# Performance work log

Measured on AMD Instinct MI355X. Metric: run time of the kernel, lower is better.

The kernel has to match this reference:

```python
import jax, jax.numpy as jnp
import numpy as np

N_NODES = 50000
N_EDGES = 800000
N_GRAPHS = 64
EPS = 1e-5


def glorot(key, shape):
    fan_in, fan_out = shape[0], shape[1]
    lim = np.sqrt(6.0 / (fan_in + fan_out))
    return jax.random.uniform(key, shape, jnp.float32, -lim, lim)


def setup_inputs() -> dict:
    key = jax.random.key(0)
    ks = jax.random.split(key, 12)
    x = jax.random.normal(ks[0], (N_NODES, 1), jnp.float32)
    edge_index = jax.random.randint(ks[1], (2, N_EDGES), 0, N_NODES, jnp.int64)
    batch = jnp.sort(jax.random.randint(ks[2], (N_NODES,), 0, N_GRAPHS, jnp.int64))
    dims = [(1, 256), (256, 256), (256, 128)]
    params = {}
    for i, (di, do) in enumerate(dims):
        params[f"Wl{i}"] = glorot(ks[3 + 3 * i], (di, do))          # neighbor (lin_l) weight
        params[f"b{i}"] = jnp.zeros((do,), jnp.float32)              # lin_l bias
        params[f"Wr{i}"] = glorot(ks[4 + 3 * i], (di, do))           # root (lin_r) weight
    params["gamma"] = jnp.ones((128,), jnp.float32)
    params["beta"] = jnp.zeros((128,), jnp.float32)
    return {"x": x, "edge_index": edge_index, "batch": batch, **params}


def _sage_conv(x, src, dst, deg_inv, Wl, b, Wr):
    # mean-aggregate messages x[src] at dst, then lin_l(agg) + lin_r(x)
    agg = jax.ops.segment_sum(x[src], dst, num_segments=N_NODES) * deg_inv
    return agg @ Wl + b + x @ Wr


def reference(x, edge_index, batch, Wl0, b0, Wr0, Wl1, b1, Wr1, Wl2, b2, Wr2, gamma, beta):
    src, dst = edge_index[0], edge_index[1]
    deg = jax.ops.segment_sum(jnp.ones((N_EDGES,), x.dtype), dst, num_segments=N_NODES)
    deg_inv = (1.0 / jnp.maximum(deg, 1.0))[:, None]

    h = _sage_conv(x, src, dst, deg_inv, Wl0, b0, Wr0)
    h = jax.nn.relu(h)  # dropout is identity in eval mode
    h = _sage_conv(h, src, dst, deg_inv, Wl1, b1, Wr1)
    h = jax.nn.relu(h)
    h = _sage_conv(h, src, dst, deg_inv, Wl2, b2, Wr2)

    # global mean pool over graphs
    gsum = jax.ops.segment_sum(h, batch, num_segments=N_GRAPHS)
    gcnt = jax.ops.segment_sum(jnp.ones((N_NODES,), h.dtype), batch, num_segments=N_GRAPHS)
    g = gsum / jnp.maximum(gcnt, 1.0)[:, None]

    # LayerNorm over feature dim
    mu = jnp.mean(g, axis=-1, keepdims=True)
    var = jnp.var(g, axis=-1, keepdims=True)
    return (g - mu) * jax.lax.rsqrt(var + EPS) * gamma + beta
```

## Files before the change

### kernel.cpp

```cpp
#include <hip/hip_runtime.h>
#include <stdint.h>

#define NN 50000
#define NE 800000
#define NG 64
#define F1 256
#define NBK 196
#define NBS 392
#define EPB 2048
#define SCB 391
#define PB 256
#define PCH 196

typedef __bf16 bf16x8 __attribute__((ext_vector_type(8)));
typedef float f32x4 __attribute__((ext_vector_type(4)));

__device__ __forceinline__ float bf2f(unsigned int u) {
  union { float f; unsigned int i; } v; v.i = (u & 0xffffu) << 16; return v.f;
}
__device__ __forceinline__ unsigned short f2bf(float f) {
  union { float f; unsigned int i; } v; v.f = f;
  unsigned int r = v.i + 0x7fffu + ((v.i >> 16) & 1u);
  return (unsigned short)(r >> 16);
}
__device__ __forceinline__ float asf(unsigned int u) {
  union { unsigned int u; float f; } v; v.u = u; return v.f;
}
__device__ __forceinline__ unsigned int asu(float f) {
  union { float f; unsigned int u; } v; v.f = f; return v.u;
}

__global__ void k_bhist(const int* __restrict__ ei, int* __restrict__ btot_d,
                        int* __restrict__ btot_s) {
  __shared__ int lhd[NBK];
  __shared__ int lhs[NBS];
  for (int i = threadIdx.x; i < NBK; i += 256) lhd[i] = 0;
  for (int i = threadIdx.x; i < NBS; i += 256) lhs[i] = 0;
  __syncthreads();
  for (int e = blockIdx.x * blockDim.x + threadIdx.x; e < NE; e += gridDim.x * blockDim.x) {
    atomicAdd(&lhs[ei[e] >> 7], 1);
    atomicAdd(&lhd[ei[NE + e] >> 8], 1);
  }
  __syncthreads();
  for (int i = threadIdx.x; i < NBK; i += 256) atomicAdd(&btot_d[i], lhd[i]);
  for (int i = threadIdx.x; i < NBS; i += 256) atomicAdd(&btot_s[i], lhs[i]);
}

__global__ void k_bscan(const int* __restrict__ btot_d, const int* __restrict__ btot_s,
                        int* __restrict__ bbase, int* __restrict__ bcur,
                        int* __restrict__ sbase, int* __restrict__ scur,
                        int* __restrict__ rowp) {
  __shared__ int buf[512];
  int t = threadIdx.x;
  int v = (t < NBK) ? btot_d[t] : 0;
  buf[t] = v;
  __syncthreads();
  for (int off = 1; off < 512; off <<= 1) {
    int o = (t >= off) ? buf[t - off] : 0;
    __syncthreads();
    buf[t] += o;
    __syncthreads();
  }
  if (t < NBK) { bbase[t] = buf[t] - v; bcur[t] = buf[t] - v; }
  if (t == NBK - 1) bbase[NBK] = buf[t];
  __syncthreads();
  int v2 = (t < NBS) ? btot_s[t] : 0;
  buf[t] = v2;
  __syncthreads();
  for (int off = 1; off < 512; off <<= 1) {
    int o = (t >= off) ? buf[t - off] : 0;
    __syncthreads();
    buf[t] += o;
    __syncthreads();
  }
  if (t < NBS) { sbase[t] = buf[t] - v2; scur[t] = buf[t] - v2; }
  if (t == NBS - 1) sbase[NBS] = buf[t];
  if (t == 0) rowp[NN] = NE;
}

__global__ __launch_bounds__(256) void k_bscatter(
    const int* __restrict__ ei, const float* __restrict__ x,
    int* __restrict__ bcur, int* __restrict__ scur,
    uint2* __restrict__ recs, unsigned int* __restrict__ srecs) {
  __shared__ int lhd[NBK]; __shared__ int gbd[NBK];
  __shared__ int lhs[NBS]; __shared__ int gbs[NBS];
  int b = blockIdx.x, tid = threadIdx.x;
  int e0 = b * EPB;
  for (int i = tid; i < NBK; i += 256) lhd[i] = 0;
  for (int i = tid; i < NBS; i += 256) lhs[i] = 0;
  __syncthreads();
  unsigned int meta[8]; float xv[8]; int lofd[8]; int bkd[8]; int lofs[8]; int bks[8];
#pragma unroll
  for (int i = 0; i < 8; ++i) {
    int e = e0 + i * 256 + tid;
    bkd[i] = -1;
    if (e < NE) {
      int s = ei[e], d = ei[NE + e];
      bkd[i] = d >> 8; bks[i] = s >> 7;
      meta[i] = (unsigned int)s | ((unsigned int)d << 16);
      xv[i] = x[s];
      lofd[i] = atomicAdd(&lhd[bkd[i]], 1);
      lofs[i] = atomicAdd(&lhs[bks[i]], 1);
    }
  }
  __syncthreads();
  for (int i = tid; i < NBK; i += 256) gbd[i] = atomicAdd(&bcur[i], lhd[i]);
  for (int i = tid; i < NBS; i += 256) gbs[i] = atomicAdd(&scur[i], lhs[i]);
  __syncthreads();
#pragma unroll
  for (int i = 0; i < 8; ++i) {
    if (bkd[i] >= 0) {
      recs[gbd[bkd[i]] + lofd[i]] = make_uint2(meta[i], asu(xv[i]));
      unsigned int s = meta[i] & 0xFFFFu, d = meta[i] >> 16;
      srecs[gbs[bks[i]] + lofs[i]] = d | ((s & 127u) << 16);
    }
  }
}

__global__ __launch_bounds__(256) void k_csr(
    const uint2* __restrict__ recs, const int* __restrict__ bbase,
    const float* __restrict__ x, const int* __restrict__ batch,
    int* __restrict__ rowp, float2* __restrict__ ax,
    int* __restrict__ colx, uint2* __restrict__ dg) {
  __shared__ int cnt[256];
  __shared__ int sc[256];
  __shared__ float xs[256];
  int b = blockIdx.x, tid = threadIdx.x;
  int eb = bbase[b], ee = bbase[b + 1];
  cnt[tid] = 0;
  xs[tid] = 0.0f;
  __syncthreads();
  for (int e = eb + tid; e < ee; e += 256) {
    uint2 r = recs[e];
    int dl = (r.x >> 16) & 255;
    atomicAdd(&cnt[dl], 1);
    atomicAdd(&xs[dl], asf(r.y));
  }
  __syncthreads();
  sc[tid] = cnt[tid];
  __syncthreads();
  for (int off = 1; off < 256; off <<= 1) {
    int o = (tid >= off) ? sc[tid - off] : 0;
    __syncthreads();
    sc[tid] += o;
    __syncthreads();
  }
  int excl = sc[tid] - cnt[tid];
  int i = b * 256 + tid;
  float dinv = 1.0f / fmaxf((float)cnt[tid], 1.0f);
  if (i < NN) {
    rowp[i] = eb + excl;
    ax[i] = make_float2(xs[tid] * dinv, x[i]);
    dg[i] = make_uint2(asu(dinv), (unsigned int)batch[i]);
  }
  __syncthreads();
  sc[tid] = excl;
  __syncthreads();
  for (int e = eb + tid; e < ee; e += 256) {
    uint2 r = recs[e];
    int dl = (r.x >> 16) & 255;
    int s = r.x & 0xFFFF;
    int slot = atomicAdd(&sc[dl], 1);
    colx[eb + slot] = s;
  }
}

__global__ __launch_bounds__(256) void k_csc(
    const unsigned int* __restrict__ srecs, const int* __restrict__ sbase,
    const uint2* __restrict__ dg, float* __restrict__ wg) {
  __shared__ float wgrow[128][64];
  int b = blockIdx.x, tid = threadIdx.x;
  f32x4 zz = {0.f, 0.f, 0.f, 0.f};
  for (int j = tid; j < 2048; j += 256) ((f32x4*)wgrow)[j] = zz;
  __syncthreads();
  int eb = sbase[b], ee = sbase[b + 1];
  for (int e = eb + tid; e < ee; e += 256) {
    unsigned int r = srecs[e];
    int d = r & 0xFFFF;
    int sl = (r >> 16) & 127;
    uint2 t = dg[d];
    atomicAdd(&wgrow[sl][t.y], asf(t.x));
  }
  __syncthreads();
  int s0 = b * 128;
  for (int j = tid; j < 2048; j += 256) {
    int row = j >> 4, col = (j & 15) * 4;
    int s = s0 + row;
    if (s < NN) *(f32x4*)&wg[(size_t)s * NG + col] = *(const f32x4*)&wgrow[row][col];
  }
}

__global__ void k_cnt(const int* __restrict__ batch, int* __restrict__ cnt) {
  int g = threadIdx.x;
  if (g >= NG) return;
  int lo = 0, hi = NN;
  while (lo < hi) { int m = (lo + hi) >> 1; if (batch[m] < g) lo = m + 1; else hi = m; }
  int a = lo;
  lo = 0; hi = NN;
  while (lo < hi) { int m = (lo + hi) >> 1; if (batch[m] < g + 1) lo = m + 1; else hi = m; }
  cnt[g] = lo - a;
}

__global__ void k_axe(const int* __restrict__ colx, const float2* __restrict__ ax,
                      float2* __restrict__ axe) {
  int e = blockIdx.x * blockDim.x + threadIdx.x;
  if (e >= NE) return;
  axe[e] = ax[colx[e]];
}

__global__ void k_wprep(const float* __restrict__ Wl1, const float* __restrict__ Wr1,
                        unsigned short* __restrict__ wcat) {
  int t = blockIdx.x * blockDim.x + threadIdx.x;
  if (t >= 256 * 512) return;
  int n = t >> 9, k = t & 511;
  float v = (k < 256) ? Wl1[k * 256 + n] : Wr1[(k - 256) * 256 + n];
  wcat[t] = f2bf(v);
}

__global__ __launch_bounds__(256) void k_agg2(
    const float2* __restrict__ axe, const int* __restrict__ rowp,
    const float* __restrict__ Wl0, const float* __restrict__ b0,
    const float* __restrict__ Wr0, unsigned short* __restrict__ aggb) {
  int wid = threadIdx.x >> 6, lane = threadIdx.x & 63;
  int gw = blockIdx.x * 4 + wid;
  int tw = gridDim.x * 4;
  float wl[4], wr[4], bb[4];
#pragma unroll
  for (int k = 0; k < 4; ++k) {
    wl[k] = Wl0[lane * 4 + k];
    wr[k] = Wr0[lane * 4 + k];
    bb[k] = b0[lane * 4 + k];
  }
  for (int d = gw; d < NN; d += tw) {
    int beg = rowp[d], end = rowp[d + 1];
    float a[4] = {0.f, 0.f, 0.f, 0.f};
    float c[4] = {0.f, 0.f, 0.f, 0.f};
    int e = beg;
    for (; e + 3 < end; e += 4) {
      float2 v0 = axe[e], v1 = axe[e + 1], v2 = axe[e + 2], v3 = axe[e + 3];
#pragma unroll
      for (int k = 0; k < 4; ++k) {
        a[k] += fmaxf(fmaf(v0.x, wl[k], fmaf(v0.y, wr[k], bb[k])), 0.0f);
        c[k] += fmaxf(fmaf(v1.x, wl[k], fmaf(v1.y, wr[k], bb[k])), 0.0f);
        a[k] += fmaxf(fmaf(v2.x, wl[k], fmaf(v2.y, wr[k], bb[k])), 0.0f);
        c[k] += fmaxf(fmaf(v3.x, wl[k], fmaf(v3.y, wr[k], bb[k])), 0.0f);
      }
    }
    for (; e < end; ++e) {
      float2 v0 = axe[e];
#pragma unroll
      for (int k = 0; k < 4; ++k)
        a[k] += fmaxf(fmaf(v0.x, wl[k], fmaf(v0.y, wr[k], bb[k])), 0.0f);
    }
    float dinv = 1.0f / fmaxf((float)(end - beg), 1.0f);
    uint2 o;
    o.x = (unsigned int)f2bf((a[0] + c[0]) * dinv) | ((unsigned int)f2bf((a[1] + c[1]) * dinv) << 16);
    o.y = (unsigned int)f2bf((a[2] + c[2]) * dinv) | ((unsigned int)f2bf((a[3] + c[3]) * dinv) << 16);
    *(uint2*)(aggb + (size_t)d * F1 + lane * 4) = o;
  }
}

#define BM 128
#define BN 128
#define BK 32

__global__ __launch_bounds__(256) void k_gemm1(
    const unsigned short* __restrict__ aggb, const float2* __restrict__ ax,
    const unsigned short* __restrict__ wcat,
    const float* __restrict__ Wl0, const float* __restrict__ b0,
    const float* __restrict__ Wr0, const float* __restrict__ b1,
    unsigned short* __restrict__ h1b) {
  __shared__ unsigned short As[2][BM][BK];
  __shared__ unsigned short Bs[2][BN][BK];
  __shared__ float wl0s[256], wr0s[256], b0s[256];
  int bm = blockIdx.x, ct = blockIdx.y;
  int tid = threadIdx.x;
  int wid = tid >> 6, lane = tid & 63;
  int wr = wid >> 1, wc = wid & 1;
  int rc = lane & 15, kh = lane >> 4;
  int r0 = bm * BM;
  int srow = tid >> 1;
  int sslot = tid & 1;

  wl0s[tid] = Wl0[tid];
  wr0s[tid] = Wr0[tid];
  b0s[tid] = b0[tid];

  int rA = r0 + srow;
  bool rAok = rA < NN;
  float2 axv = rAok ? ax[rA] : make_float2(0.f, 0.f);

  f32x4 acc[4][4] = {};
  int4 ra0, ra1, rb0, rb1;

#define LOAD_A(kt)                                                             \
  do {                                                                         \
    ra0 = make_int4(0, 0, 0, 0); ra1 = make_int4(0, 0, 0, 0);                  \
    if (rAok) {                                                                \
      const int4* s_ = (const int4*)(aggb + (size_t)rA * F1 + (kt) * BK + sslot * 16); \
      ra0 = s_[0]; ra1 = s_[1];                                                \
    }                                                                          \
  } while (0)

#define LOAD_B(kt)                                                             \
  do {                                                                         \
    const int4* t_ = (const int4*)(wcat + (size_t)(ct * BN + srow) * 512 + (kt) * BK + sslot * 16); \
    rb0 = t_[0]; rb1 = t_[1];                                                  \
  } while (0)

#define COMP_A(kt)                                                             \
  do {                                                                         \
    int j0_ = ((kt) - 8) * BK + sslot * 16;                                    \
    unsigned int w_[8];                                                        \
    _Pragma("unroll") for (int q = 0; q < 8; ++q) {                            \
      int j_ = j0_ + 2 * q;                                                    \
      float f0_ = fmaxf(fmaf(axv.x, wl0s[j_], fmaf(axv.y, wr0s[j_], b0s[j_])), 0.0f); \
      float f1_ = fmaxf(fmaf(axv.x, wl0s[j_ + 1], fmaf(axv.y, wr0s[j_ + 1], b0s[j_ + 1])), 0.0f); \
      w_[q] = (unsigned int)f2bf(f0_) | ((unsigned int)f2bf(f1_) << 16);       \
    }                                                                          \
    ra0 = make_int4(w_[0], w_[1], w_[2], w_[3]);                               \
    ra1 = make_int4(w_[4], w_[5], w_[6], w_[7]);                               \
  } while (0)

#define WRITE_AB(buf)                                                          \
  do {                                                                         \
    int sw_ = (srow >> 1) & 3;                                                 \
    int ws0_ = (2 * sslot) ^ sw_;                                              \
    int ws1_ = (2 * sslot + 1) ^ sw_;                                          \
    *(int4*)&As[buf][srow][ws0_ * 8] = ra0;                                    \
    *(int4*)&As[buf][srow][ws1_ * 8] = ra1;                                    \
    *(int4*)&Bs[buf][srow][ws0_ * 8] = rb0;                                    \
    *(int4*)&Bs[buf][srow][ws1_ * 8] = rb1;                                    \
  } while (0)

  LOAD_B(0);
  LOAD_A(0);
  WRITE_AB(0);
  __syncthreads();
  int cur = 0;
  for (int kt = 0; kt < 16; ++kt) {
    if (kt < 15) {
      LOAD_B(kt + 1);
      if (kt + 1 < 8) LOAD_A(kt + 1);
    }
    bf16x8 af[4], bfr[4];
#pragma unroll
    for (int mf = 0; mf < 4; ++mf) {
      int row = wr * 64 + mf * 16 + rc;
      int sl = kh ^ ((row >> 1) & 3);
      af[mf] = *(const bf16x8*)&As[cur][row][sl * 8];
    }
#pragma unroll
    for (int nf = 0; nf < 4; ++nf) {
      int row = wc * 64 + nf * 16 + rc;
      int sl = kh ^ ((row >> 1) & 3);
      bfr[nf] = *(const bf16x8*)&Bs[cur][row][sl * 8];
    }
#pragma unroll
    for (int nf = 0; nf < 4; ++nf)
#pragma unroll
      for (int mf = 0; mf < 4; ++mf)
        acc[nf][mf] = __builtin_amdgcn_mfma_f32_16x16x32_bf16(bfr[nf], af[mf], acc[nf][mf], 0, 0, 0);
    if (kt < 15) {
      if (kt + 1 >= 8) COMP_A(kt + 1);
      WRITE_AB(cur ^ 1);
    }
    __syncthreads();
    cur ^= 1;
  }
#undef LOAD_A
#undef LOAD_B
#undef COMP_A
#undef WRITE_AB

#pragma unroll
  for (int nf = 0; nf < 4; ++nf) {
    int c0 = ct * BN + wc * 64 + nf * 16 + kh * 4;
    float4 bb = *(const float4*)(b1 + c0);
#pragma unroll
    for (int mf = 0; mf < 4; ++mf) {
      int r = r0 + wr * 64 + mf * 16 + rc;
      if (r < NN) {
        f32x4 v = acc[nf][mf];
        unsigned int lo = (unsigned int)f2bf(fmaxf(v[0] + bb.x, 0.0f)) |
                          ((unsigned int)f2bf(fmaxf(v[1] + bb.y, 0.0f)) << 16);
        unsigned int hi = (unsigned int)f2bf(fmaxf(v[2] + bb.z, 0.0f)) |
                          ((unsigned int)f2bf(fmaxf(v[3] + bb.w, 0.0f)) << 16);
        *(uint2*)(h1b + (size_t)r * F1 + c0) = make_uint2(lo, hi);
      }
    }
  }
}

__global__ __launch_bounds__(512) void k_pool2(
    const unsigned short* __restrict__ h1b, const float* __restrict__ wg,
    const int* __restrict__ batch, float* __restrict__ zpart,
    float* __restrict__ p1) {
  __shared__ float h1s[32][256];
  __shared__ float wgs[32][64];
  int b = blockIdx.x, tid = threadIdx.x;
  int s0 = b * PCH;
  int lim = min(s0 + PCH, NN);
  int gq = tid >> 6;
  int fq = tid & 63;
  int col = tid & 255;
  int half = tid >> 8;
  f32x4 acc[8] = {};
  float pac = 0.0f;
  int curg = -1;
  for (int t0 = 0; t0 < PCH; t0 += 32) {
    int base = s0 + t0;
    {
      int r = tid >> 4;
      int c0 = (tid & 15) * 16;
      int s = base + r;
      uint4 va = make_uint4(0, 0, 0, 0), vb = make_uint4(0, 0, 0, 0);
      if (s < lim) {
        va = *(const uint4*)(h1b + (size_t)s * F1 + c0);
        vb = *(const uint4*)(h1b + (size_t)s * F1 + c0 + 8);
      }
      float* dst = &h1s[r][c0];
      unsigned int u[8] = {va.x, va.y, va.z, va.w, vb.x, vb.y, vb.z, vb.w};
#pragma unroll
      for (int q = 0; q < 8; ++q) {
        dst[2 * q] = bf2f(u[q]);
        union { float f; unsigned int i; } hi; hi.i = u[q] & 0xffff0000u;
        dst[2 * q + 1] = hi.f;
      }
    }
    {
      int r = tid >> 4;
      int c0 = (tid & 15) * 4;
      int s = base + r;
      float4 v = make_float4(0.f, 0.f, 0.f, 0.f);
      if (s < lim) v = *(const float4*)(wg + (size_t)s * NG + c0);
      *(float4*)&wgs[r][c0] = v;
    }
    __syncthreads();
    int rows = min(32, lim - base);
    for (int k = 0; k < rows; ++k) {
      f32x4 hv = *(const f32x4*)&h1s[k][fq << 2];
      f32x4 w0 = *(const f32x4*)&wgs[k][gq << 3];
      f32x4 w1 = *(const f32x4*)&wgs[k][(gq << 3) + 4];
#pragma unroll
      for (int i = 0; i < 4; ++i) acc[i] += w0[i] * hv;
#pragma unroll
      for (int i = 0; i < 4; ++i) acc[4 + i] += w1[i] * hv;
    }
    int kend = min(half * 16 + 16, rows);
    for (int k = half * 16; k < kend; ++k) {
      int g = batch[base + k];
      if (g != curg) {
        if (curg >= 0) atomicAdd(&p1[curg * F1 + col], pac);
        pac = 0.0f;
        curg = g;
      }
      pac += h1s[k][col];
    }
    __syncthreads();
  }
  if (curg >= 0) atomicAdd(&p1[curg * F1 + col], pac);
  float* zp = zpart + ((size_t)b * 64 + gq * 8) * F1 + (fq << 2);
#pragma unroll
  for (int i = 0; i < 8; ++i) *(f32x4*)(zp + (size_t)i * F1) = acc[i];
}

__global__ void k_zred(const float* __restrict__ zpart, float* __restrict__ z) {
  int g = blockIdx.x, q = blockIdx.y, t = threadIdx.x;
  float a = 0.0f;
  for (int b = q * 64; b < q * 64 + 64; ++b)
    a += zpart[((size_t)b * 64 + g) * F1 + t];
  atomicAdd(&z[g * F1 + t], a);
}

__global__ void k_final(const float* __restrict__ z, const float* __restrict__ p1,
                        const int* __restrict__ cnt,
                        const float* __restrict__ Wl2, const float* __restrict__ b2,
                        const float* __restrict__ Wr2, const float* __restrict__ gamma,
                        const float* __restrict__ beta, float* __restrict__ out) {
  __shared__ float s1[128], s2[128];
  int g = blockIdx.x, j = threadIdx.x;
  float invc = 1.0f / fmaxf((float)cnt[g], 1.0f);
  float acc = 0.0f;
  for (int k = 0; k < 256; ++k) {
    acc += z[g * 256 + k] * Wl2[k * 128 + j] + p1[g * 256 + k] * Wr2[k * 128 + j];
  }
  acc = acc * invc + b2[j];
  s1[j] = acc; s2[j] = acc * acc;
  __syncthreads();
  for (int off = 64; off > 0; off >>= 1) {
    if (j < off) { s1[j] += s1[j + off]; s2[j] += s2[j + off]; }
    __syncthreads();
  }
  float mu = s1[0] / 128.0f;
  float var = s2[0] / 128.0f - mu * mu;
  out[g * 128 + j] = (acc - mu) * rsqrtf(var + 1e-5f) * gamma[j] + beta[j];
}

extern "C" void kernel_launch(void* const* d_in, const int* in_sizes, int n_in,
                              void* d_out, int out_size, void* d_ws, size_t ws_size,
                              hipStream_t stream) {
  const float* x = (const float*)d_in[0];
  const int* ei = (const int*)d_in[1];
  const int* batch = (const int*)d_in[2];
  const float* Wl0 = (const float*)d_in[3];
  const float* b0 = (const float*)d_in[4];
  const float* Wr0 = (const float*)d_in[5];
  const float* Wl1 = (const float*)d_in[6];
  const float* b1 = (const float*)d_in[7];
  const float* Wr1 = (const float*)d_in[8];
  const float* Wl2 = (const float*)d_in[9];
  const float* b2 = (const float*)d_in[10];
  const float* Wr2 = (const float*)d_in[11];
  const float* gamma = (const float*)d_in[12];
  const float* beta = (const float*)d_in[13];
  float* out = (float*)d_out;

  char* p = (char*)d_ws;
  auto alloc = [&](size_t bytes) {
    char* r = p;
    p += (bytes + 511) & ~(size_t)511;
    return r;
  };
  unsigned short* h1b = (unsigned short*)alloc((size_t)NN * F1 * 2);
  unsigned short* aggb = (unsigned short*)alloc((size_t)NN * F1 * 2);
  float2* axe = (float2*)alloc((size_t)NE * 8);
  int* rowp = (int*)alloc((size_t)(NN + 1) * 4);
  float2* ax = (float2*)alloc((size_t)NN * 8);
  uint2* dg = (uint2*)alloc((size_t)NN * 8);
  int* cnt = (int*)alloc((size_t)NG * 4);
  float* z = (float*)alloc((size_t)NG * F1 * 4);
  float* p1 = (float*)alloc((size_t)NG * F1 * 4);
  unsigned short* wcat = (unsigned short*)alloc((size_t)256 * 512 * 2);
  int* btot_d = (int*)alloc((size_t)NBK * 4);
  int* btot_s = (int*)alloc((size_t)NBS * 4);
  int* bbase = (int*)alloc((size_t)(NBK + 1) * 4);
  int* bcur = (int*)alloc((size_t)NBK * 4);
  int* sbase = (int*)alloc((size_t)(NBS + 1) * 4);
  int* scur = (int*)alloc((size_t)NBS * 4);
  float* wg = (float*)alloc((size_t)NN * NG * 4);
  uint2* recs = (uint2*)aggb;
  unsigned int* srecs = (unsigned int*)(aggb + (size_t)NE * 4);
  int* colx = (int*)(aggb + (size_t)NE * 6);
  float* zpart = (float*)aggb;

  hipMemsetAsync(btot_d, 0, (size_t)NBK * 4, stream);
  hipMemsetAsync(btot_s, 0, (size_t)NBS * 4, stream);
  hipMemsetAsync(p1, 0, (size_t)NG * F1 * 4, stream);
  hipMemsetAsync(z, 0, (size_t)NG * F1 * 4, stream);

  k_bhist<<<256, 256, 0, stream>>>(ei, btot_d, btot_s);
  k_bscan<<<1, 512, 0, stream>>>(btot_d, btot_s, bbase, bcur, sbase, scur, rowp);
  k_bscatter<<<SCB, 256, 0, stream>>>(ei, x, bcur, scur, recs, srecs);
  k_csr<<<NBK, 256, 0, stream>>>(recs, bbase, x, batch, rowp, ax, colx, dg);
  k_csc<<<NBS, 256, 0, stream>>>(srecs, sbase, dg, wg);
  k_cnt<<<1, 64, 0, stream>>>(batch, cnt);
  k_axe<<<(NE + 255) / 256, 256, 0, stream>>>(colx, ax, axe);
  k_wprep<<<(256 * 512 + 255) / 256, 256, 0, stream>>>(Wl1, Wr1, wcat);
  k_agg2<<<2048, 256, 0, stream>>>(axe, rowp, Wl0, b0, Wr0, aggb);
  dim3 gg(391, 2);
  k_gemm1<<<gg, 256, 0, stream>>>(aggb, ax, wcat, Wl0, b0, Wr0, b1, h1b);
  k_pool2<<<PB, 512, 0, stream>>>(h1b, wg, batch, zpart, p1);
  dim3 zg(NG, 4);
  k_zred<<<zg, 256, 0, stream>>>(zpart, z);
  k_final<<<NG, 128, 0, stream>>>(z, p1, cnt, Wl2, b2, Wr2, gamma, beta, out);
}
```

Before: 218.6 us.

## Fuse root-pooling into GEMM epilogue and run graph-weight pooling on MFMA

The GEMM epilogue now writes h1 transposed (feature-major, swizzled through LDS) and accumulates the per-graph root sum p1 directly with shuffles and atomics, removing that work from the pool kernel. The per-node graph weights from k_csc are stored transposed as a split bf16 hi/lo pair so the z = wg^T·h1 reduction can run as a bf16 MFMA GEMM in a new k_poolmm kernel, replacing the scalar FMA k_pool2. This targets the FP32 scalar pooling cost and the extra pass over h1. In exchange it adds a padded node dimension, extra epilogue atomics, and h1 rounding to bf16 in the pooling product.

Measured after the change: 223.2 us. 2.1% more time.

```diff
diff --git a/kernel.cpp b/kernel.cpp
--- a/kernel.cpp
+++ b/kernel.cpp
@@ -5,12 +5,13 @@
 #define NE 800000
 #define NG 64
 #define F1 256
+#define NNP 50176
 #define NBK 196
 #define NBS 392
 #define EPB 2048
 #define SCB 391
-#define PB 256
-#define PCH 196
+#define PCHUNKS 112
+#define PKC 448
 
 typedef __bf16 bf16x8 __attribute__((ext_vector_type(8)));
 typedef float f32x4 __attribute__((ext_vector_type(4)));
@@ -167,11 +168,10 @@
 
 __global__ __launch_bounds__(256) void k_csc(
     const unsigned int* __restrict__ srecs, const int* __restrict__ sbase,
-    const uint2* __restrict__ dg, float* __restrict__ wg) {
-  __shared__ float wgrow[128][64];
+    const uint2* __restrict__ dg, unsigned int* __restrict__ wgT2u) {
+  __shared__ float wgrow[128 * 65];
   int b = blockIdx.x, tid = threadIdx.x;
-  f32x4 zz = {0.f, 0.f, 0.f, 0.f};
-  for (int j = tid; j < 2048; j += 256) ((f32x4*)wgrow)[j] = zz;
+  for (int i = tid; i < 128 * 65; i += 256) wgrow[i] = 0.0f;
   __syncthreads();
   int eb = sbase[b], ee = sbase[b + 1];
   for (int e = eb + tid; e < ee; e += 256) {
@@ -179,14 +179,19 @@
     int d = r & 0xFFFF;
     int sl = (r >> 16) & 127;
     uint2 t = dg[d];
-    atomicAdd(&wgrow[sl][t.y], asf(t.x));
-  }
-  __syncthreads();
-  int s0 = b * 128;
-  for (int j = tid; j < 2048; j += 256) {
-    int row = j >> 4, col = (j & 15) * 4;
-    int s = s0 + row;
-    if (s < NN) *(f32x4*)&wg[(size_t)s * NG + col] = *(const f32x4*)&wgrow[row][col];
+    atomicAdd(&wgrow[sl * 65 + t.y], asf(t.x));
+  }
+  __syncthreads();
+  int s0u = b * 64;
+  int k = tid & 63;
+  for (int rr = 0; rr < 16; ++rr) {
+    int g = rr * 4 + (tid >> 6);
+    float w0 = wgrow[(2 * k) * 65 + g];
+    float w1 = wgrow[(2 * k + 1) * 65 + g];
+    unsigned short h0 = f2bf(w0), h1v = f2bf(w1);
+    unsigned short l0 = f2bf(w0 - bf2f(h0)), l1 = f2bf(w1 - bf2f(h1v));
+    wgT2u[(size_t)g * (NNP / 2) + s0u + k] = (unsigned int)h0 | ((unsigned int)h1v << 16);
+    wgT2u[(size_t)(64 + g) * (NNP / 2) + s0u + k] = (unsigned int)l0 | ((unsigned int)l1 << 16);
   }
 }
 
@@ -269,10 +274,17 @@
     const unsigned short* __restrict__ wcat,
     const float* __restrict__ Wl0, const float* __restrict__ b0,
     const float* __restrict__ Wr0, const float* __restrict__ b1,
-    unsigned short* __restrict__ h1b) {
-  __shared__ unsigned short As[2][BM][BK];
-  __shared__ unsigned short Bs[2][BN][BK];
-  __shared__ float wl0s[256], wr0s[256], b0s[256];
+    const int* __restrict__ batch, float* __restrict__ p1,
+    unsigned short* __restrict__ h1T) {
+  __shared__ unsigned char SMEM[35840];
+  typedef unsigned short ush;
+  ush (*As)[BM][BK] = (ush (*)[BM][BK])SMEM;
+  ush (*Bs)[BN][BK] = (ush (*)[BN][BK])(SMEM + 16384);
+  float* wl0s = (float*)(SMEM + 32768);
+  float* wr0s = wl0s + 256;
+  float* b0s = wl0s + 512;
+  ush* Ts = (ush*)SMEM;
+
   int bm = blockIdx.x, ct = blockIdx.y;
   int tid = threadIdx.x;
   int wid = tid >> 6, lane = tid & 63;
@@ -373,103 +385,107 @@
 #undef COMP_A
 #undef WRITE_AB
 
+  int gv[4];
+#pragma unroll
+  for (int mf = 0; mf < 4; ++mf) {
+    int s = r0 + wr * 64 + mf * 16 + rc;
+    gv[mf] = (s < NN) ? batch[s] : -1;
+  }
+  int g0 = 0, g1 = -1;
+  if (r0 < NN) {
+    g0 = batch[r0];
+    g1 = batch[min(r0 + 127, NN - 1)];
+  }
+
 #pragma unroll
   for (int nf = 0; nf < 4; ++nf) {
-    int c0 = ct * BN + wc * 64 + nf * 16 + kh * 4;
-    float4 bb = *(const float4*)(b1 + c0);
+    int c0l = wc * 64 + nf * 16 + kh * 4;
+    float4 bbq = *(const float4*)(b1 + ct * BN + c0l);
+    float bbv[4] = {bbq.x, bbq.y, bbq.z, bbq.w};
+    float v[4][4];
+#pragma unroll
+    for (int mf = 0; mf < 4; ++mf)
+#pragma unroll
+      for (int j = 0; j < 4; ++j)
+        v[mf][j] = fmaxf(acc[nf][mf][j] + bbv[j], 0.0f);
 #pragma unroll
     for (int mf = 0; mf < 4; ++mf) {
-      int r = r0 + wr * 64 + mf * 16 + rc;
-      if (r < NN) {
-        f32x4 v = acc[nf][mf];
-        unsigned int lo = (unsigned int)f2bf(fmaxf(v[0] + bb.x, 0.0f)) |
-                          ((unsigned int)f2bf(fmaxf(v[1] + bb.y, 0.0f)) << 16);
-        unsigned int hi = (unsigned int)f2bf(fmaxf(v[2] + bb.z, 0.0f)) |
-                          ((unsigned int)f2bf(fmaxf(v[3] + bb.w, 0.0f)) << 16);
-        *(uint2*)(h1b + (size_t)r * F1 + c0) = make_uint2(lo, hi);
+      int s_loc = wr * 64 + mf * 16 + rc;
+#pragma unroll
+      for (int j = 0; j < 4; ++j) {
+        int f_loc = c0l + j;
+        Ts[f_loc * 128 + (s_loc ^ ((f_loc & 7) << 3))] = f2bf(v[mf][j]);
       }
     }
-  }
-}
-
-__global__ __launch_bounds__(512) void k_pool2(
-    const unsigned short* __restrict__ h1b, const float* __restrict__ wg,
-    const int* __restrict__ batch, float* __restrict__ zpart,
-    float* __restrict__ p1) {
-  __shared__ float h1s[32][256];
-  __shared__ float wgs[32][64];
-  int b = blockIdx.x, tid = threadIdx.x;
-  int s0 = b * PCH;
-  int lim = min(s0 + PCH, NN);
-  int gq = tid >> 6;
-  int fq = tid & 63;
-  int col = tid & 255;
-  int half = tid >> 8;
+    for (int g = g0; g <= g1; ++g) {
+#pragma unroll
+      for (int j = 0; j < 4; ++j) {
+        float s = 0.f;
+#pragma unroll
+        for (int mf = 0; mf < 4; ++mf) s += (gv[mf] == g) ? v[mf][j] : 0.f;
+        s += __shfl_xor(s, 1); s += __shfl_xor(s, 2);
+        s += __shfl_xor(s, 4); s += __shfl_xor(s, 8);
+        if (rc == 0 && s != 0.f) atomicAdd(&p1[g * F1 + ct * BN + c0l + j], s);
+      }
+    }
+  }
+  __syncthreads();
+  {
+    int f_loc = tid >> 1;
+    int sh = (tid & 1) * 64;
+    size_t rowoff = (size_t)(ct * BN + f_loc) * NNP + (size_t)bm * BM;
+#pragma unroll
+    for (int q = 0; q < 8; ++q) {
+      int s_l = sh + q * 8;
+      int4 vv = *(const int4*)&Ts[f_loc * 128 + (s_l ^ ((f_loc & 7) << 3))];
+      *(int4*)(h1T + rowoff + s_l) = vv;
+    }
+  }
+}
+
+__global__ __launch_bounds__(512) void k_poolmm(
+    const unsigned short* __restrict__ h1T, const unsigned short* __restrict__ wgT2,
+    float* __restrict__ zpart) {
+  int bid = blockIdx.x;
+  int c = bid % PCHUNKS, fh = bid / PCHUNKS;
+  int tid = threadIdx.x;
+  int w = tid >> 6, lane = tid & 63, rc = lane & 15, kh = lane >> 4;
+  size_t soff = (size_t)c * PKC + kh * 8;
+  const unsigned short* bp = h1T + (size_t)(fh * 128 + w * 16 + rc) * NNP + soff;
+  const unsigned short* ap = wgT2 + (size_t)rc * NNP + soff;
   f32x4 acc[8] = {};
-  float pac = 0.0f;
-  int curg = -1;
-  for (int t0 = 0; t0 < PCH; t0 += 32) {
-    int base = s0 + t0;
-    {
-      int r = tid >> 4;
-      int c0 = (tid & 15) * 16;
-      int s = base + r;
-      uint4 va = make_uint4(0, 0, 0, 0), vb = make_uint4(0, 0, 0, 0);
-      if (s < lim) {
-        va = *(const uint4*)(h1b + (size_t)s * F1 + c0);
-        vb = *(const uint4*)(h1b + (size_t)s * F1 + c0 + 8);
-      }
-      float* dst = &h1s[r][c0];
-      unsigned int u[8] = {va.x, va.y, va.z, va.w, vb.x, vb.y, vb.z, vb.w};
-#pragma unroll
-      for (int q = 0; q < 8; ++q) {
-        dst[2 * q] = bf2f(u[q]);
-        union { float f; unsigned int i; } hi; hi.i = u[q] & 0xffff0000u;
-        dst[2 * q + 1] = hi.f;
-      }
-    }
-    {
-      int r = tid >> 4;
-      int c0 = (tid & 15) * 4;
-      int s = base + r;
-      float4 v = make_float4(0.f, 0.f, 0.f, 0.f);
-      if (s < lim) v = *(const float4*)(wg + (size_t)s * NG + c0);
-      *(float4*)&wgs[r][c0] = v;
-    }
-    __syncthreads();
-    int rows = min(32, lim - base);
-    for (int k = 0; k < rows; ++k) {
-      f32x4 hv = *(const f32x4*)&h1s[k][fq << 2];
-      f32x4 w0 = *(const f32x4*)&wgs[k][gq << 3];
-      f32x4 w1 = *(const f32x4*)&wgs[k][(gq << 3) + 4];
-#pragma unroll
-      for (int i = 0; i < 4; ++i) acc[i] += w0[i] * hv;
-#pragma unroll
-      for (int i = 0; i < 4; ++i) acc[4 + i] += w1[i] * hv;
-    }
-    int kend = min(half * 16 + 16, rows);
-    for (int k = half * 16; k < kend; ++k) {
-      int g = batch[base + k];
-      if (g != curg) {
-        if (curg >= 0) atomicAdd(&p1[curg * F1 + col], pac);
-        pac = 0.0f;
-        curg = g;
-      }
-      pac += h1s[k][col];
-    }
-    __syncthreads();
-  }
-  if (curg >= 0) atomicAdd(&p1[curg * F1 + col], pac);
-  float* zp = zpart + ((size_t)b * 64 + gq * 8) * F1 + (fq << 2);
-#pragma unroll
-  for (int i = 0; i < 8; ++i) *(f32x4*)(zp + (size_t)i * F1) = acc[i];
+  bf16x8 a0[8], a1[8], bA, bB;
+#define PLOADS(da, db, ks)                                                     \
+  do {                                                                         \
+    db = *(const bf16x8*)(bp + (ks) * 32);                                     \
+    _Pragma("unroll") for (int mt = 0; mt < 8; ++mt)                           \
+      da[mt] = *(const bf16x8*)(ap + (size_t)mt * 16 * NNP + (ks) * 32);       \
+  } while (0)
+  PLOADS(a0, bA, 0);
+  for (int ks = 0; ks < 14; ks += 2) {
+    PLOADS(a1, bB, ks + 1);
+#pragma unroll
+    for (int mt = 0; mt < 8; ++mt)
+      acc[mt] = __builtin_amdgcn_mfma_f32_16x16x32_bf16(a0[mt], bA, acc[mt], 0, 0, 0);
+    if (ks + 2 < 14) PLOADS(a0, bA, ks + 2);
+#pragma unroll
+    for (int mt = 0; mt < 8; ++mt)
+      acc[mt] = __builtin_amdgcn_mfma_f32_16x16x32_bf16(a1[mt], bB, acc[mt], 0, 0, 0);
+  }
+#undef PLOADS
+  float* zp = zpart + ((size_t)c * 128) * F1 + fh * 128 + w * 16 + rc;
+#pragma unroll
+  for (int mt = 0; mt < 8; ++mt)
+#pragma unroll
+    for (int r = 0; r < 4; ++r)
+      zp[(size_t)(mt * 16 + kh * 4 + r) * F1] = acc[mt][r];
 }
 
 __global__ void k_zred(const float* __restrict__ zpart, float* __restrict__ z) {
   int g = blockIdx.x, q = blockIdx.y, t = threadIdx.x;
   float a = 0.0f;
-  for (int b = q * 64; b < q * 64 + 64; ++b)
-    a += zpart[((size_t)b * 64 + g) * F1 + t];
+  for (int c = q * 28; c < q * 28 + 28; ++c)
+    a += zpart[((size_t)c * 128 + g) * F1 + t] + zpart[((size_t)c * 128 + 64 + g) * F1 + t];
   atomicAdd(&z[g * F1 + t], a);
 }
 
@@ -522,7 +538,7 @@
     p += (bytes + 511) & ~(size_t)511;
     return r;
   };
-  unsigned short* h1b = (unsigned short*)alloc((size_t)NN * F1 * 2);
+  unsigned short* h1T = (unsigned short*)alloc((size_t)F1 * NNP * 2);
   unsigned short* aggb = (unsigned short*)alloc((size_t)NN * F1 * 2);
   float2* axe = (float2*)alloc((size_t)NE * 8);
   int* rowp = (int*)alloc((size_t)(NN + 1) * 4);
@@ -538,7 +554,7 @@
   int* bcur = (int*)alloc((size_t)NBK * 4);
   int* sbase = (int*)alloc((size_t)(NBS + 1) * 4);
   int* scur = (int*)alloc((size_t)NBS * 4);
-  float* wg = (float*)alloc((size_t)NN * NG * 4);
+  unsigned short* wgT2 = (unsigned short*)alloc((size_t)128 * NNP * 2);
   uint2* recs = (uint2*)aggb;
   unsigned int* srecs = (unsigned int*)(aggb + (size_t)NE * 4);
   int* colx = (int*)(aggb + (size_t)NE * 6);
@@ -553,14 +569,14 @@
   k_bscan<<<1, 512, 0, stream>>>(btot_d, btot_s, bbase, bcur, sbase, scur, rowp);
   k_bscatter<<<SCB, 256, 0, stream>>>(ei, x, bcur, scur, recs, srecs);
   k_csr<<<NBK, 256, 0, stream>>>(recs, bbase, x, batch, rowp, ax, colx, dg);
-  k_csc<<<NBS, 256, 0, stream>>>(srecs, sbase, dg, wg);
+  k_csc<<<NBS, 256, 0, stream>>>(srecs, sbase, dg, (unsigned int*)wgT2);
   k_cnt<<<1, 64, 0, stream>>>(batch, cnt);
   k_axe<<<(NE + 255) / 256, 256, 0, stream>>>(colx, ax, axe);
   k_wprep<<<(256 * 512 + 255) / 256, 256, 0, stream>>>(Wl1, Wr1, wcat);
   k_agg2<<<2048, 256, 0, stream>>>(axe, rowp, Wl0, b0, Wr0, aggb);
-  dim3 gg(391, 2);
-  k_gemm1<<<gg, 256, 0, stream>>>(aggb, ax, wcat, Wl0, b0, Wr0, b1, h1b);
-  k_pool2<<<PB, 512, 0, stream>>>(h1b, wg, batch, zpart, p1);
+  dim3 gg(392, 2);
+  k_gemm1<<<gg, 256, 0, stream>>>(aggb, ax, wcat, Wl0, b0, Wr0, b1, batch, p1, h1T);
+  k_poolmm<<<2 * PCHUNKS, 512, 0, stream>>>(h1T, wgT2, zpart);
   dim3 zg(NG, 4);
   k_zred<<<zg, 256, 0, stream>>>(zpart, z);
   k_final<<<NG, 128, 0, stream>>>(z, p1, cnt, Wl2, b2, Wr2, gamma, beta, out);
```
